# Optimization experiments

Measured on AMD Instinct MI355X. Metric: run time of the kernel, lower is better.

Reference implementation:

```python
import jax, jax.numpy as jnp
import numpy as np

B, T, U, QS, MS = 64, 2048, 512, 512, 512

def setup_inputs() -> dict:
    key = jax.random.key(0)
    k1, k2, k3, k4, k5 = jax.random.split(key, 5)
    query = jax.random.normal(k1, (B, QS), dtype=jnp.float32)
    keys = jax.random.normal(k2, (B, T, MS), dtype=jnp.float32)
    # torch nn.Linear weights: [out, in], no bias
    Wq = jax.random.normal(k3, (U, QS), dtype=jnp.float32) * (1.0 / np.sqrt(QS))
    Wm = jax.random.normal(k4, (U, MS), dtype=jnp.float32) * (1.0 / np.sqrt(MS))
    Wa = jax.random.normal(k5, (1, U), dtype=jnp.float32) * (1.0 / np.sqrt(U))
    return {"query": query, "keys": keys, "Wq": Wq, "Wm": Wm, "Wa": Wa}

def reference(query, keys, Wq, Wm, Wa):
    # processed_query: [B, U]
    pq = jnp.einsum('bq,uq->bu', query, Wq)
    # values: [B, T, U]
    vals = jnp.einsum('btm,um->btu', keys, Wm)
    # alignment score: [B, T]
    score = jnp.einsum('btu,u->bt', jnp.tanh(pq[:, None, :] + vals), Wa[0])
    weight = jax.nn.softmax(score, axis=-1)            # [B, T]
    total_context = jnp.einsum('bt,btm->bm', weight, keys)  # [B, MS]
    return (total_context, score)
```

## Files before the change

kernel.cpp:

```cpp
#include <hip/hip_runtime.h>
#include <cstdint>
#include <cstddef>

#define Bn 64
#define Tn 2048
#define Un 512
#define QSn 512
#define MSn 512
#define TCH 64
#define NCH 32
#define NKT 16

using f32x16 = __attribute__((ext_vector_type(16))) float;
using bf16x8 = __attribute__((ext_vector_type(8))) short;

__device__ __forceinline__ unsigned short f2bf(float x) {
    unsigned int u = __float_as_uint(x);
    u += 0x7FFFu + ((u >> 16) & 1u);
    return (unsigned short)(u >> 16);
}

__device__ __forceinline__ unsigned int pk2bf(float lo, float hi) {
    unsigned int r;
    asm("v_cvt_pk_bf16_f32 %0, %1, %2" : "=v"(r) : "v"(lo), "v"(hi));
    return r;
}

__device__ __forceinline__ bf16x8 cvt8(float4 a, float4 b) {
    union { unsigned int u[4]; bf16x8 v; } r;
    r.u[0] = pk2bf(a.x, a.y);
    r.u[1] = pk2bf(a.z, a.w);
    r.u[2] = pk2bf(b.x, b.y);
    r.u[3] = pk2bf(b.z, b.w);
    return r.v;
}

__device__ __forceinline__ float tanh_fast(float x) {
    float e = exp2f(x * 2.885390043258667f);
    return 1.f - 2.f * __builtin_amdgcn_rcpf(e + 1.f);
}

#define GLOAD(G, L) __builtin_amdgcn_global_load_lds( \
    (const __attribute__((address_space(1))) void*)(G), \
    (__attribute__((address_space(3))) void*)(L), 16, 0, 0)

__global__ __launch_bounds__(256) void cvt_kernel(const float* __restrict__ src,
                                                  unsigned short* __restrict__ dst) {
    int i = blockIdx.x * 256 + threadIdx.x;
    float4 v = *(const float4*)(src + (size_t)i * 4);
    ushort4 h = { f2bf(v.x), f2bf(v.y), f2bf(v.z), f2bf(v.w) };
    *(ushort4*)&dst[(size_t)i * 4] = h;
}

__global__ __launch_bounds__(128) void pq_kernel(const float* __restrict__ query,
                                                 const float* __restrict__ Wq,
                                                 float* __restrict__ pq) {
    __shared__ float ql[QSn];
    const int b = blockIdx.x;
    const int quad = blockIdx.y;
    const int tid = threadIdx.x;
    for (int i = tid; i < QSn; i += 128) ql[i] = query[(size_t)b * QSn + i];
    __syncthreads();
    const int u = quad * 128 + tid;
    const float* w = Wq + (size_t)u * QSn;
    float a0 = 0.f, a1 = 0.f;
    #pragma unroll 4
    for (int k = 0; k < QSn; k += 8) {
        float4 w0 = *(const float4*)(w + k);
        float4 w1 = *(const float4*)(w + k + 4);
        float4 q0 = *(const float4*)(ql + k);
        float4 q1 = *(const float4*)(ql + k + 4);
        a0 += w0.x * q0.x + w0.y * q0.y + w0.z * q0.z + w0.w * q0.w;
        a1 += w1.x * q1.x + w1.y * q1.y + w1.z * q1.z + w1.w * q1.w;
    }
    pq[(size_t)b * Un + u] = a0 + a1;
}

__global__ __launch_bounds__(256, 2) void fused_kernel(const float* __restrict__ keys,
                                                       const unsigned short* __restrict__ WmB,
                                                       const float* __restrict__ pq,
                                                       const float* __restrict__ Wa,
                                                       float* __restrict__ score_out,
                                                       float* __restrict__ pm,
                                                       float* __restrict__ pl,
                                                       float* __restrict__ pctx) {
    __shared__ __align__(16) unsigned short Ah[2][TCH * 32];
    __shared__ __align__(16) unsigned short Bh[4][2][128 * 32];
    __shared__ float sc_lds[4][TCH];
    __shared__ float stot[TCH];
    __shared__ float wexp[TCH];

    const int tid = threadIdx.x;
    const int lane = tid & 63;
    const int w = tid >> 6;
    const int lc = lane & 31;
    const int l5 = lane >> 5;
    const int b = blockIdx.y;
    const int chunk = blockIdx.x;
    const int t0 = chunk * TCH;

    const int arow = tid >> 2;
    const int akg = tid & 3;
    const int awof = (tid >> 3) * 64 +
                     ((((akg << 1) | (arow & 1)) ^ ((tid >> 3) & 7)) * 8);
    const float* gA = keys + ((size_t)b * Tn + t0 + arow) * MSn + akg * 8;

    const int bg = (lane & 7) ^ ((lane >> 3) & 7);
    const size_t bloff = (size_t)(((lane >> 3) << 1) | (bg & 1)) * MSn + (bg >> 1) * 8;
    const unsigned short* gBw = WmB + (size_t)(w * 128) * MSn + bloff;
    char* bD = (char*)&Bh[w][0][0];

    f32x16 acc[2][4];
    #pragma unroll
    for (int mf = 0; mf < 2; ++mf)
        #pragma unroll
        for (int nf = 0; nf < 4; ++nf)
            #pragma unroll
            for (int r = 0; r < 16; ++r) acc[mf][nf][r] = 0.f;

    float4 a0, a1;

    a0 = *(const float4*)(gA);
    a1 = *(const float4*)(gA + 4);
    __builtin_amdgcn_sched_barrier(0);
    #pragma unroll
    for (int j = 0; j < 8; ++j)
        GLOAD(gBw + (size_t)j * 16 * MSn, bD + j * 1024);
    __builtin_amdgcn_sched_barrier(0);
    asm volatile("s_waitcnt vmcnt(8)" ::: "memory");
    __builtin_amdgcn_sched_barrier(0);
    *(bf16x8*)&Ah[0][awof] = cvt8(a0, a1);
    asm volatile("s_waitcnt lgkmcnt(0)" ::: "memory");
    __builtin_amdgcn_s_barrier();
    __builtin_amdgcn_sched_barrier(0);

    #pragma unroll
    for (int kt = 0; kt < NKT; ++kt) {
        const int cur = kt & 1;

        if (kt < NKT - 1) {
            const float* g = gA + (kt + 1) * 32;
            a0 = *(const float4*)(g);
            a1 = *(const float4*)(g + 4);
            __builtin_amdgcn_sched_barrier(0);
            const unsigned short* gb = gBw + (kt + 1) * 32;
            char* bdn = bD + (cur ^ 1) * 8192;
            #pragma unroll
            for (int j = 0; j < 8; ++j)
                GLOAD(gb + (size_t)j * 16 * MSn, bdn + j * 1024);
            __builtin_amdgcn_sched_barrier(0);
            asm volatile("s_waitcnt vmcnt(10)" ::: "memory");
        } else {
            asm volatile("s_waitcnt vmcnt(0)" ::: "memory");
        }
        __builtin_amdgcn_sched_barrier(0);

        {
            const unsigned short* lA = &Ah[cur][0];
            const unsigned short* lB = &Bh[w][cur][0];
            #pragma unroll
            for (int ks = 0; ks < 2; ++ks) {
                bf16x8 af[2];
                #pragma unroll
                for (int mf = 0; mf < 2; ++mf) {
                    int r = mf * 32 + lc;
                    int gp = (((ks * 2 + l5) << 1) | (r & 1)) ^ ((r >> 1) & 7);
                    af[mf] = *(const bf16x8*)&lA[(r >> 1) * 64 + gp * 8];
                }
                #pragma unroll
                for (int nf = 0; nf < 4; ++nf) {
                    int ru = nf * 32 + lc;
                    int gp = (((ks * 2 + l5) << 1) | (ru & 1)) ^ ((ru >> 1) & 7);
                    bf16x8 bfr = *(const bf16x8*)&lB[(ru >> 1) * 64 + gp * 8];
                    acc[0][nf] = __builtin_amdgcn_mfma_f32_32x32x16_bf16(af[0], bfr, acc[0][nf], 0, 0, 0);
                    acc[1][nf] = __builtin_amdgcn_mfma_f32_32x32x16_bf16(af[1], bfr, acc[1][nf], 0, 0, 0);
                }
            }
        }

        if (kt < NKT - 1) {
            asm volatile("s_waitcnt vmcnt(8)" ::: "memory");
            __builtin_amdgcn_sched_barrier(0);
            *(bf16x8*)&Ah[cur ^ 1][awof] = cvt8(a0, a1);
            asm volatile("s_waitcnt lgkmcnt(0)" ::: "memory");
            __builtin_amdgcn_s_barrier();
            __builtin_amdgcn_sched_barrier(0);
        }
    }

    float pqv[4], wav[4];
    #pragma unroll
    for (int nf = 0; nf < 4; ++nf) {
        int u = w * 128 + nf * 32 + lc;
        pqv[nf] = pq[(size_t)b * Un + u];
        wav[nf] = Wa[u];
    }
    #pragma unroll
    for (int mf = 0; mf < 2; ++mf) {
        #pragma unroll
        for (int r = 0; r < 16; ++r) {
            float s = 0.f;
            #pragma unroll
            for (int nf = 0; nf < 4; ++nf)
                s += tanh_fast(acc[mf][nf][r] + pqv[nf]) * wav[nf];
            s += __shfl_xor(s, 16);
            s += __shfl_xor(s, 8);
            s += __shfl_xor(s, 4);
            s += __shfl_xor(s, 2);
            s += __shfl_xor(s, 1);
            if (lc == 0)
                sc_lds[w][mf * 32 + (r & 3) + 8 * (r >> 2) + 4 * l5] = s;
        }
    }
    __syncthreads();
    if (tid < TCH) {
        float v = (sc_lds[0][tid] + sc_lds[1][tid]) + (sc_lds[2][tid] + sc_lds[3][tid]);
        stot[tid] = v;
        score_out[(size_t)b * Tn + t0 + tid] = v;
    }
    __syncthreads();

    if (tid < 64) {
        float v = stot[tid];
        float mx = v;
        #pragma unroll
        for (int off = 32; off; off >>= 1) mx = fmaxf(mx, __shfl_xor(mx, off));
        float e = __expf(v - mx);
        wexp[tid] = e;
        float sum = e;
        #pragma unroll
        for (int off = 32; off; off >>= 1) sum += __shfl_xor(sum, off);
        if (tid == 0) {
            pm[b * NCH + chunk] = mx;
            pl[b * NCH + chunk] = sum;
        }
    }
    __syncthreads();

    const int c0 = tid * 2;
    const float* kp = keys + ((size_t)b * Tn + t0) * MSn + c0;
    float cx = 0.f, cy = 0.f;
    #pragma unroll 8
    for (int t = 0; t < TCH; ++t) {
        float2 kv = *(const float2*)(kp + (size_t)t * MSn);
        float wt = wexp[t];
        cx += wt * kv.x;
        cy += wt * kv.y;
    }
    float2 cacc = { cx, cy };
    *(float2*)&pctx[((size_t)(b * NCH + chunk)) * MSn + c0] = cacc;
}

__global__ __launch_bounds__(512) void merge_kernel(const float* __restrict__ pm,
                                                    const float* __restrict__ pl,
                                                    const float* __restrict__ pctx,
                                                    float* __restrict__ ctx) {
    __shared__ float sm[NCH], sl[NCH];
    const int b = blockIdx.x, tid = threadIdx.x;
    if (tid < NCH) {
        sm[tid] = pm[b * NCH + tid];
        sl[tid] = pl[b * NCH + tid];
    }
    __syncthreads();
    float M = -1e30f;
    #pragma unroll
    for (int c = 0; c < NCH; ++c) M = fmaxf(M, sm[c]);
    float L = 0.f;
    #pragma unroll
    for (int c = 0; c < NCH; ++c) L += sl[c] * __expf(sm[c] - M);
    const float inv = 1.f / L;
    float acc = 0.f;
    #pragma unroll
    for (int c = 0; c < NCH; ++c)
        acc += __expf(sm[c] - M) * pctx[((size_t)(b * NCH + c)) * MSn + tid];
    ctx[(size_t)b * MSn + tid] = acc * inv;
}

extern "C" void kernel_launch(void* const* d_in, const int* in_sizes, int n_in,
                              void* d_out, int out_size, void* d_ws, size_t ws_size,
                              hipStream_t stream) {
    const float* query = (const float*)d_in[0];
    const float* keys  = (const float*)d_in[1];
    const float* Wq    = (const float*)d_in[2];
    const float* Wm    = (const float*)d_in[3];
    const float* Wa    = (const float*)d_in[4];

    float* ctx_out   = (float*)d_out;
    float* score_out = (float*)d_out + (size_t)Bn * MSn;

    char* ws = (char*)d_ws;
    float* ws_pq   = (float*)(ws);
    unsigned short* ws_wmbf = (unsigned short*)(ws + 131072);
    float* ws_pm   = (float*)(ws + 655360);
    float* ws_pl   = (float*)(ws + 663552);
    float* ws_pctx = (float*)(ws + 671744);

    cvt_kernel<<<(Un * MSn / 4) / 256, 256, 0, stream>>>(Wm, ws_wmbf);
    pq_kernel<<<dim3(Bn, 4), 128, 0, stream>>>(query, Wq, ws_pq);
    fused_kernel<<<dim3(NCH, Bn), 256, 0, stream>>>(keys, ws_wmbf, ws_pq, Wa,
                                                    score_out, ws_pm, ws_pl, ws_pctx);
    merge_kernel<<<Bn, 512, 0, stream>>>(ws_pm, ws_pl, ws_pctx, ctx_out);
}
```

Baseline: 187.2 us.

## Share Wm tiles across waves and split K-step into two half-U phases

Wm tiles now live in four shared buffers of 256 U-rows, each loaded cooperatively by all waves, in place of per-wave private buffers. Each K-step is split into two phases, one per U half, each ending in a barrier. Keys are prefetched two K-steps ahead. The goal is finer-grained overlap of global loads with MFMA work and earlier loading of pq/Wa, at the cost of an extra block barrier per K-step and tighter vmcnt bookkeeping.

```diff
diff --git a/kernel.cpp b/kernel.cpp
--- a/kernel.cpp
+++ b/kernel.cpp
@@ -43,6 +43,13 @@
 #define GLOAD(G, L) __builtin_amdgcn_global_load_lds( \
     (const __attribute__((address_space(1))) void*)(G), \
     (__attribute__((address_space(3))) void*)(L), 16, 0, 0)
+
+#define SB() __builtin_amdgcn_sched_barrier(0)
+
+#define PHASE_END(N) do { \
+    asm volatile("s_waitcnt vmcnt(" #N ") lgkmcnt(0)" ::: "memory"); \
+    __builtin_amdgcn_s_barrier(); \
+    SB(); } while (0)
 
 __global__ __launch_bounds__(256) void cvt_kernel(const float* __restrict__ src,
                                                   unsigned short* __restrict__ dst) {
@@ -85,7 +92,7 @@
                                                        float* __restrict__ pl,
                                                        float* __restrict__ pctx) {
     __shared__ __align__(16) unsigned short Ah[2][TCH * 32];
-    __shared__ __align__(16) unsigned short Bh[4][2][128 * 32];
+    __shared__ __align__(16) unsigned short Bh[4][256 * 32];
     __shared__ float sc_lds[4][TCH];
     __shared__ float stot[TCH];
     __shared__ float wexp[TCH];
@@ -99,110 +106,134 @@
     const int chunk = blockIdx.x;
     const int t0 = chunk * TCH;
 
-    const int arow = tid >> 2;
+    const int ar = tid >> 2;
     const int akg = tid & 3;
     const int awof = (tid >> 3) * 64 +
-                     ((((akg << 1) | (arow & 1)) ^ ((tid >> 3) & 7)) * 8);
-    const float* gA = keys + ((size_t)b * Tn + t0 + arow) * MSn + akg * 8;
+                     ((((akg << 1) | (ar & 1)) ^ ((tid >> 3) & 7)) * 8);
+    const float* gA = keys + ((size_t)b * Tn + t0 + ar) * MSn + akg * 8;
 
     const int bg = (lane & 7) ^ ((lane >> 3) & 7);
-    const size_t bloff = (size_t)(((lane >> 3) << 1) | (bg & 1)) * MSn + (bg >> 1) * 8;
-    const unsigned short* gBw = WmB + (size_t)(w * 128) * MSn + bloff;
-    char* bD = (char*)&Bh[w][0][0];
-
-    f32x16 acc[2][4];
-    #pragma unroll
-    for (int mf = 0; mf < 2; ++mf)
-        #pragma unroll
-        for (int nf = 0; nf < 4; ++nf)
+    const int brow2 = ((lane >> 3) << 1) | (bg & 1);
+    const unsigned short* gBt = WmB + (size_t)(w * 64 + brow2) * MSn + (bg >> 1) * 8;
+
+    #define STAGE_B(KT, UH, BUF) do { \
+        const unsigned short* s_ = gBt + (size_t)((UH) * 256) * MSn + (KT) * 32; \
+        char* d_ = (char*)&Bh[BUF][0] + w * 4096; \
+        GLOAD(s_,                    d_); \
+        GLOAD(s_ + (size_t)16 * MSn, d_ + 1024); \
+        GLOAD(s_ + (size_t)32 * MSn, d_ + 2048); \
+        GLOAD(s_ + (size_t)48 * MSn, d_ + 3072); } while (0)
+
+    f32x16 acc[2][2][2];
+    #pragma unroll
+    for (int uh = 0; uh < 2; ++uh)
+        #pragma unroll
+        for (int mf = 0; mf < 2; ++mf)
             #pragma unroll
-            for (int r = 0; r < 16; ++r) acc[mf][nf][r] = 0.f;
-
-    float4 a0, a1;
-
-    a0 = *(const float4*)(gA);
-    a1 = *(const float4*)(gA + 4);
-    __builtin_amdgcn_sched_barrier(0);
-    #pragma unroll
-    for (int j = 0; j < 8; ++j)
-        GLOAD(gBw + (size_t)j * 16 * MSn, bD + j * 1024);
-    __builtin_amdgcn_sched_barrier(0);
-    asm volatile("s_waitcnt vmcnt(8)" ::: "memory");
-    __builtin_amdgcn_sched_barrier(0);
-    *(bf16x8*)&Ah[0][awof] = cvt8(a0, a1);
+            for (int nf = 0; nf < 2; ++nf)
+                #pragma unroll
+                for (int r = 0; r < 16; ++r) acc[uh][mf][nf][r] = 0.f;
+
+    bf16x8 af[2][2];
+
+    #define READ_AF(CUR) do { \
+        const unsigned short* lA_ = &Ah[CUR][0]; \
+        _Pragma("unroll") \
+        for (int ks = 0; ks < 2; ++ks) \
+            _Pragma("unroll") \
+            for (int mf = 0; mf < 2; ++mf) { \
+                int r_ = mf * 32 + lc; \
+                int gp_ = (((ks * 2 + l5) << 1) | (r_ & 1)) ^ ((r_ >> 1) & 7); \
+                af[mf][ks] = *(const bf16x8*)&lA_[(r_ >> 1) * 64 + gp_ * 8]; \
+            } } while (0)
+
+    #define MFMA_PH(UH, BUF) do { \
+        const unsigned short* lB_ = &Bh[BUF][0]; \
+        _Pragma("unroll") \
+        for (int ks = 0; ks < 2; ++ks) { \
+            bf16x8 bfr0, bfr1; \
+            { int ru_ = w * 64 + lc; \
+              int gp_ = (((ks * 2 + l5) << 1) | (ru_ & 1)) ^ ((ru_ >> 1) & 7); \
+              bfr0 = *(const bf16x8*)&lB_[(ru_ >> 1) * 64 + gp_ * 8]; } \
+            { int ru_ = w * 64 + 32 + lc; \
+              int gp_ = (((ks * 2 + l5) << 1) | (ru_ & 1)) ^ ((ru_ >> 1) & 7); \
+              bfr1 = *(const bf16x8*)&lB_[(ru_ >> 1) * 64 + gp_ * 8]; } \
+            acc[UH][0][0] = __builtin_amdgcn_mfma_f32_32x32x16_bf16(af[0][ks], bfr0, acc[UH][0][0], 0, 0, 0); \
+            acc[UH][0][1] = __builtin_amdgcn_mfma_f32_32x32x16_bf16(af[0][ks], bfr1, acc[UH][0][1], 0, 0, 0); \
+            acc[UH][1][0] = __builtin_amdgcn_mfma_f32_32x32x16_bf16(af[1][ks], bfr0, acc[UH][1][0], 0, 0, 0); \
+            acc[UH][1][1] = __builtin_amdgcn_mfma_f32_32x32x16_bf16(af[1][ks], bfr1, acc[UH][1][1], 0, 0, 0); \
+        } } while (0)
+
+    float pqv[2][2], wav[2][2];
+    float4 s0a, s0b, s1a, s1b;
+
+    #pragma unroll
+    for (int uh = 0; uh < 2; ++uh)
+        #pragma unroll
+        for (int nf = 0; nf < 2; ++nf) {
+            int u = uh * 256 + w * 64 + nf * 32 + lc;
+            pqv[uh][nf] = pq[(size_t)b * Un + u];
+            wav[uh][nf] = Wa[u];
+        }
+    SB();
+    float4 p0 = *(const float4*)(gA);
+    float4 p1 = *(const float4*)(gA + 4);
+    SB();
+    STAGE_B(0, 0, 0);
+    SB();
+    s1a = *(const float4*)(gA + 32);
+    s1b = *(const float4*)(gA + 36);
+    SB();
+    STAGE_B(0, 1, 1);
+    SB();
+    asm volatile("s_waitcnt vmcnt(6)" ::: "memory");
+    SB();
+    *(bf16x8*)&Ah[0][awof] = cvt8(p0, p1);
     asm volatile("s_waitcnt lgkmcnt(0)" ::: "memory");
     __builtin_amdgcn_s_barrier();
-    __builtin_amdgcn_sched_barrier(0);
+    SB();
 
     #pragma unroll
     for (int kt = 0; kt < NKT; ++kt) {
-        const int cur = kt & 1;
-
+        if (kt < NKT - 1) { STAGE_B(kt + 1, 0, ((kt + 1) & 1) << 1); SB(); }
+        if (kt < NKT - 2) {
+            const float* g = gA + (kt + 2) * 32;
+            if ((kt & 1) == 0) { s0a = *(const float4*)(g); s0b = *(const float4*)(g + 4); }
+            else               { s1a = *(const float4*)(g); s1b = *(const float4*)(g + 4); }
+            SB();
+        }
+        READ_AF(kt & 1);
+        MFMA_PH(0, (kt & 1) << 1);
+        if (kt < NKT - 2)       PHASE_END(6);
+        else if (kt == NKT - 2) PHASE_END(4);
+        else                    PHASE_END(0);
+
+        if (kt < NKT - 1) { STAGE_B(kt + 1, 1, (((kt + 1) & 1) << 1) | 1); SB(); }
+        MFMA_PH(1, ((kt & 1) << 1) | 1);
         if (kt < NKT - 1) {
-            const float* g = gA + (kt + 1) * 32;
-            a0 = *(const float4*)(g);
-            a1 = *(const float4*)(g + 4);
-            __builtin_amdgcn_sched_barrier(0);
-            const unsigned short* gb = gBw + (kt + 1) * 32;
-            char* bdn = bD + (cur ^ 1) * 8192;
-            #pragma unroll
-            for (int j = 0; j < 8; ++j)
-                GLOAD(gb + (size_t)j * 16 * MSn, bdn + j * 1024);
-            __builtin_amdgcn_sched_barrier(0);
-            asm volatile("s_waitcnt vmcnt(10)" ::: "memory");
-        } else {
-            asm volatile("s_waitcnt vmcnt(0)" ::: "memory");
-        }
-        __builtin_amdgcn_sched_barrier(0);
-
-        {
-            const unsigned short* lA = &Ah[cur][0];
-            const unsigned short* lB = &Bh[w][cur][0];
-            #pragma unroll
-            for (int ks = 0; ks < 2; ++ks) {
-                bf16x8 af[2];
-                #pragma unroll
-                for (int mf = 0; mf < 2; ++mf) {
-                    int r = mf * 32 + lc;
-                    int gp = (((ks * 2 + l5) << 1) | (r & 1)) ^ ((r >> 1) & 7);
-                    af[mf] = *(const bf16x8*)&lA[(r >> 1) * 64 + gp * 8];
-                }
-                #pragma unroll
-                for (int nf = 0; nf < 4; ++nf) {
-                    int ru = nf * 32 + lc;
-                    int gp = (((ks * 2 + l5) << 1) | (ru & 1)) ^ ((ru >> 1) & 7);
-                    bf16x8 bfr = *(const bf16x8*)&lB[(ru >> 1) * 64 + gp * 8];
-                    acc[0][nf] = __builtin_amdgcn_mfma_f32_32x32x16_bf16(af[0], bfr, acc[0][nf], 0, 0, 0);
-                    acc[1][nf] = __builtin_amdgcn_mfma_f32_32x32x16_bf16(af[1], bfr, acc[1][nf], 0, 0, 0);
-                }
-            }
-        }
-
-        if (kt < NKT - 1) {
-            asm volatile("s_waitcnt vmcnt(8)" ::: "memory");
-            __builtin_amdgcn_sched_barrier(0);
-            *(bf16x8*)&Ah[cur ^ 1][awof] = cvt8(a0, a1);
-            asm volatile("s_waitcnt lgkmcnt(0)" ::: "memory");
-            __builtin_amdgcn_s_barrier();
-            __builtin_amdgcn_sched_barrier(0);
-        }
-    }
-
-    float pqv[4], wav[4];
-    #pragma unroll
-    for (int nf = 0; nf < 4; ++nf) {
-        int u = w * 128 + nf * 32 + lc;
-        pqv[nf] = pq[(size_t)b * Un + u];
-        wav[nf] = Wa[u];
-    }
+            float4 pa, pb;
+            if (((kt + 1) & 1) == 0) { pa = s0a; pb = s0b; }
+            else                     { pa = s1a; pb = s1b; }
+            *(bf16x8*)&Ah[(kt + 1) & 1][awof] = cvt8(pa, pb);
+        }
+        if (kt < NKT - 2)       PHASE_END(6);
+        else if (kt == NKT - 2) PHASE_END(4);
+        else { asm volatile("s_waitcnt lgkmcnt(0)" ::: "memory"); __builtin_amdgcn_s_barrier(); SB(); }
+    }
+    #undef STAGE_B
+    #undef READ_AF
+    #undef MFMA_PH
+
     #pragma unroll
     for (int mf = 0; mf < 2; ++mf) {
         #pragma unroll
         for (int r = 0; r < 16; ++r) {
             float s = 0.f;
             #pragma unroll
-            for (int nf = 0; nf < 4; ++nf)
-                s += tanh_fast(acc[mf][nf][r] + pqv[nf]) * wav[nf];
+            for (int uh = 0; uh < 2; ++uh)
+                #pragma unroll
+                for (int nf = 0; nf < 2; ++nf)
+                    s += tanh_fast(acc[uh][mf][nf][r] + pqv[uh][nf]) * wav[uh][nf];
             s += __shfl_xor(s, 16);
             s += __shfl_xor(s, 8);
             s += __shfl_xor(s, 4);
```

After: 191.0 us. 2.0% more time.

## Split fused kernel across eight waves with shared B tile and simpler barriers

Applied to the files above, without the earlier changes.

The fused attention-score kernel moves from 256 to 512 threads, so each of eight waves computes 64 of the U columns instead of 128. This halves per-wave accumulators and should allow higher occupancy. The hand-tuned vmcnt/sched_barrier pipelining is replaced by plain __syncthreads around a double-buffered LDS tile. Only half the threads load the A tile, and the context pass now has each thread handle one column. The risks are lost fine-grained load/compute overlap and extra block-wide barriers every k-step.

```diff
diff --git a/kernel.cpp b/kernel.cpp
--- a/kernel.cpp
+++ b/kernel.cpp
@@ -76,7 +76,7 @@
     pq[(size_t)b * Un + u] = a0 + a1;
 }
 
-__global__ __launch_bounds__(256, 2) void fused_kernel(const float* __restrict__ keys,
+__global__ __launch_bounds__(512, 4) void fused_kernel(const float* __restrict__ keys,
                                                        const unsigned short* __restrict__ WmB,
                                                        const float* __restrict__ pq,
                                                        const float* __restrict__ Wa,
@@ -85,8 +85,8 @@
                                                        float* __restrict__ pl,
                                                        float* __restrict__ pctx) {
     __shared__ __align__(16) unsigned short Ah[2][TCH * 32];
-    __shared__ __align__(16) unsigned short Bh[4][2][128 * 32];
-    __shared__ float sc_lds[4][TCH];
+    __shared__ __align__(16) unsigned short Bh[2][512 * 32];
+    __shared__ float sc_lds[8][TCH];
     __shared__ float stot[TCH];
     __shared__ float wexp[TCH];
 
@@ -99,68 +99,53 @@
     const int chunk = blockIdx.x;
     const int t0 = chunk * TCH;
 
-    const int arow = tid >> 2;
+    const int ar = tid >> 2;
     const int akg = tid & 3;
     const int awof = (tid >> 3) * 64 +
-                     ((((akg << 1) | (arow & 1)) ^ ((tid >> 3) & 7)) * 8);
-    const float* gA = keys + ((size_t)b * Tn + t0 + arow) * MSn + akg * 8;
+                     ((((akg << 1) | (ar & 1)) ^ ((tid >> 3) & 7)) * 8);
+    const float* gA = keys + ((size_t)b * Tn + t0 + ar) * MSn + akg * 8;
 
     const int bg = (lane & 7) ^ ((lane >> 3) & 7);
-    const size_t bloff = (size_t)(((lane >> 3) << 1) | (bg & 1)) * MSn + (bg >> 1) * 8;
-    const unsigned short* gBw = WmB + (size_t)(w * 128) * MSn + bloff;
-    char* bD = (char*)&Bh[w][0][0];
-
-    f32x16 acc[2][4];
+    const unsigned short* gBw = WmB +
+        (size_t)(w * 64 + (((lane >> 3) << 1) | (bg & 1))) * MSn + (bg >> 1) * 8;
+
+    f32x16 acc[2][2];
     #pragma unroll
     for (int mf = 0; mf < 2; ++mf)
         #pragma unroll
-        for (int nf = 0; nf < 4; ++nf)
+        for (int nf = 0; nf < 2; ++nf)
             #pragma unroll
             for (int r = 0; r < 16; ++r) acc[mf][nf][r] = 0.f;
 
-    float4 a0, a1;
-
-    a0 = *(const float4*)(gA);
-    a1 = *(const float4*)(gA + 4);
-    __builtin_amdgcn_sched_barrier(0);
-    #pragma unroll
-    for (int j = 0; j < 8; ++j)
-        GLOAD(gBw + (size_t)j * 16 * MSn, bD + j * 1024);
-    __builtin_amdgcn_sched_barrier(0);
-    asm volatile("s_waitcnt vmcnt(8)" ::: "memory");
-    __builtin_amdgcn_sched_barrier(0);
-    *(bf16x8*)&Ah[0][awof] = cvt8(a0, a1);
-    asm volatile("s_waitcnt lgkmcnt(0)" ::: "memory");
-    __builtin_amdgcn_s_barrier();
-    __builtin_amdgcn_sched_barrier(0);
+    {
+        char* bD = (char*)&Bh[0][0] + w * 4096;
+        #pragma unroll
+        for (int j = 0; j < 4; ++j)
+            GLOAD(gBw + (size_t)j * 16 * MSn, bD + j * 1024);
+        if (tid < 256) {
+            float4 p0 = *(const float4*)(gA);
+            float4 p1 = *(const float4*)(gA + 4);
+            *(bf16x8*)&Ah[0][awof] = cvt8(p0, p1);
+        }
+    }
 
     #pragma unroll
     for (int kt = 0; kt < NKT; ++kt) {
-        const int cur = kt & 1;
-
-        if (kt < NKT - 1) {
+        __syncthreads();
+
+        float4 p0, p1;
+        if (kt < NKT - 1 && tid < 256) {
             const float* g = gA + (kt + 1) * 32;
-            a0 = *(const float4*)(g);
-            a1 = *(const float4*)(g + 4);
-            __builtin_amdgcn_sched_barrier(0);
-            const unsigned short* gb = gBw + (kt + 1) * 32;
-            char* bdn = bD + (cur ^ 1) * 8192;
-            #pragma unroll
-            for (int j = 0; j < 8; ++j)
-                GLOAD(gb + (size_t)j * 16 * MSn, bdn + j * 1024);
-            __builtin_amdgcn_sched_barrier(0);
-            asm volatile("s_waitcnt vmcnt(10)" ::: "memory");
-        } else {
-            asm volatile("s_waitcnt vmcnt(0)" ::: "memory");
-        }
-        __builtin_amdgcn_sched_barrier(0);
+            p0 = *(const float4*)(g);
+            p1 = *(const float4*)(g + 4);
+        }
 
         {
-            const unsigned short* lA = &Ah[cur][0];
-            const unsigned short* lB = &Bh[w][cur][0];
+            const unsigned short* lA = &Ah[kt & 1][0];
+            const unsigned short* lB = &Bh[kt & 1][0];
             #pragma unroll
             for (int ks = 0; ks < 2; ++ks) {
-                bf16x8 af[2];
+                bf16x8 af[2], bfr[2];
                 #pragma unroll
                 for (int mf = 0; mf < 2; ++mf) {
                     int r = mf * 32 + lc;
@@ -168,30 +153,38 @@
                     af[mf] = *(const bf16x8*)&lA[(r >> 1) * 64 + gp * 8];
                 }
                 #pragma unroll
-                for (int nf = 0; nf < 4; ++nf) {
-                    int ru = nf * 32 + lc;
+                for (int nf = 0; nf < 2; ++nf) {
+                    int ru = w * 64 + nf * 32 + lc;
                     int gp = (((ks * 2 + l5) << 1) | (ru & 1)) ^ ((ru >> 1) & 7);
-                    bf16x8 bfr = *(const bf16x8*)&lB[(ru >> 1) * 64 + gp * 8];
-                    acc[0][nf] = __builtin_amdgcn_mfma_f32_32x32x16_bf16(af[0], bfr, acc[0][nf], 0, 0, 0);
-                    acc[1][nf] = __builtin_amdgcn_mfma_f32_32x32x16_bf16(af[1], bfr, acc[1][nf], 0, 0, 0);
+                    bfr[nf] = *(const bf16x8*)&Bh[kt & 1][(ru >> 1) * 64 + gp * 8];
+                    (void)lB;
                 }
+                #pragma unroll
+                for (int mf = 0; mf < 2; ++mf)
+                    #pragma unroll
+                    for (int nf = 0; nf < 2; ++nf)
+                        acc[mf][nf] = __builtin_amdgcn_mfma_f32_32x32x16_bf16(
+                            af[mf], bfr[nf], acc[mf][nf], 0, 0, 0);
             }
         }
 
+        __syncthreads();
+
         if (kt < NKT - 1) {
-            asm volatile("s_waitcnt vmcnt(8)" ::: "memory");
-            __builtin_amdgcn_sched_barrier(0);
-            *(bf16x8*)&Ah[cur ^ 1][awof] = cvt8(a0, a1);
-            asm volatile("s_waitcnt lgkmcnt(0)" ::: "memory");
-            __builtin_amdgcn_s_barrier();
-            __builtin_amdgcn_sched_barrier(0);
-        }
-    }
-
-    float pqv[4], wav[4];
-    #pragma unroll
-    for (int nf = 0; nf < 4; ++nf) {
-        int u = w * 128 + nf * 32 + lc;
+            char* bD = (char*)&Bh[(kt + 1) & 1][0] + w * 4096;
+            const unsigned short* gb = gBw + (kt + 1) * 32;
+            #pragma unroll
+            for (int j = 0; j < 4; ++j)
+                GLOAD(gb + (size_t)j * 16 * MSn, bD + j * 1024);
+            if (tid < 256)
+                *(bf16x8*)&Ah[(kt + 1) & 1][awof] = cvt8(p0, p1);
+        }
+    }
+
+    float pqv[2], wav[2];
+    #pragma unroll
+    for (int nf = 0; nf < 2; ++nf) {
+        int u = w * 64 + nf * 32 + lc;
         pqv[nf] = pq[(size_t)b * Un + u];
         wav[nf] = Wa[u];
     }
@@ -199,10 +192,8 @@
     for (int mf = 0; mf < 2; ++mf) {
         #pragma unroll
         for (int r = 0; r < 16; ++r) {
-            float s = 0.f;
-            #pragma unroll
-            for (int nf = 0; nf < 4; ++nf)
-                s += tanh_fast(acc[mf][nf][r] + pqv[nf]) * wav[nf];
+            float s = tanh_fast(acc[mf][0][r] + pqv[0]) * wav[0]
+                    + tanh_fast(acc[mf][1][r] + pqv[1]) * wav[1];
             s += __shfl_xor(s, 16);
             s += __shfl_xor(s, 8);
             s += __shfl_xor(s, 4);
@@ -214,7 +205,8 @@
     }
     __syncthreads();
     if (tid < TCH) {
-        float v = (sc_lds[0][tid] + sc_lds[1][tid]) + (sc_lds[2][tid] + sc_lds[3][tid]);
+        float v = ((sc_lds[0][tid] + sc_lds[1][tid]) + (sc_lds[2][tid] + sc_lds[3][tid]))
+                + ((sc_lds[4][tid] + sc_lds[5][tid]) + (sc_lds[6][tid] + sc_lds[7][tid]));
         stot[tid] = v;
         score_out[(size_t)b * Tn + t0 + tid] = v;
     }
@@ -237,18 +229,12 @@
     }
     __syncthreads();
 
-    const int c0 = tid * 2;
-    const float* kp = keys + ((size_t)b * Tn + t0) * MSn + c0;
-    float cx = 0.f, cy = 0.f;
+    const float* kp = keys + ((size_t)b * Tn + t0) * MSn + tid;
+    float cx = 0.f;
     #pragma unroll 8
-    for (int t = 0; t < TCH; ++t) {
-        float2 kv = *(const float2*)(kp + (size_t)t * MSn);
-        float wt = wexp[t];
-        cx += wt * kv.x;
-        cy += wt * kv.y;
-    }
-    float2 cacc = { cx, cy };
-    *(float2*)&pctx[((size_t)(b * NCH + chunk)) * MSn + c0] = cacc;
+    for (int t = 0; t < TCH; ++t)
+        cx += wexp[t] * kp[(size_t)t * MSn];
+    pctx[((size_t)(b * NCH + chunk)) * MSn + tid] = cx;
 }
 
 __global__ __launch_bounds__(512) void merge_kernel(const float* __restrict__ pm,
@@ -297,7 +283,7 @@
 
     cvt_kernel<<<(Un * MSn / 4) / 256, 256, 0, stream>>>(Wm, ws_wmbf);
     pq_kernel<<<dim3(Bn, 4), 128, 0, stream>>>(query, Wq, ws_pq);
-    fused_kernel<<<dim3(NCH, Bn), 256, 0, stream>>>(keys, ws_wmbf, ws_pq, Wa,
+    fused_kernel<<<dim3(NCH, Bn), 512, 0, stream>>>(keys, ws_wmbf, ws_pq, Wa,
                                                     score_out, ws_pm, ws_pl, ws_pctx);
     merge_kernel<<<Bn, 512, 0, stream>>>(ws_pm, ws_pl, ws_pctx, ctx_out);
 }
```

Measured after the change: 174.7 us. -6.7%, faster.
